# Performance work log

Hardware: AMD Instinct MI355X
Metric: run time of the kernel (lower is better)

Reference implementation:

```python
import jax, jax.numpy as jnp
import numpy as np

EPS = 1e-8
SMALL = 1e-3


def _skew(v):
    # v: [B,3] -> [B,3,3]
    vx, vy, vz = v[:, 0], v[:, 1], v[:, 2]
    z = jnp.zeros_like(vx)
    row0 = jnp.stack([z, -vz, vy], axis=-1)
    row1 = jnp.stack([vz, z, -vx], axis=-1)
    row2 = jnp.stack([-vy, vx, z], axis=-1)
    return jnp.stack([row0, row1, row2], axis=-2)


def rotmat_axis_angle_stable(aa):
    # aa: [B,3] axis*angle -> [B,3,3], Taylor-stable near theta=0
    theta = jnp.linalg.norm(aa, axis=1)
    theta2 = theta * theta + EPS
    A = jnp.sin(theta) / (theta + EPS)
    Bc = (1.0 - jnp.cos(theta)) / theta2
    th2 = theta * theta
    th4 = th2 * th2
    small = theta < SMALL
    A = jnp.where(small, 1.0 - th2 / 6.0 + th4 / 120.0, A)
    Bc = jnp.where(small, 0.5 - th2 / 24.0 + th4 / 720.0, Bc)
    K = _skew(aa)
    I = jnp.eye(3, dtype=aa.dtype)
    return I + A[:, None, None] * K + Bc[:, None, None] * jnp.matmul(K, K)


def _euler_to_rot(rpy):
    # rpy: [J,3] -> [J,3,3] (URDF origin rotations, constants)
    r, p, y = rpy[:, 0], rpy[:, 1], rpy[:, 2]
    cr, sr = jnp.cos(r), jnp.sin(r)
    cp, sp = jnp.cos(p), jnp.sin(p)
    cy, sy = jnp.cos(y), jnp.sin(y)
    row0 = jnp.stack([cy * cp, cy * sp * sr - sy * cr, cy * sp * cr + sy * sr], -1)
    row1 = jnp.stack([sy * cp, sy * sp * sr + cy * cr, sy * sp * cr - cy * sr], -1)
    row2 = jnp.stack([-sp, cp * sr, cp * cr], -1)
    return jnp.stack([row0, row1, row2], axis=-2)


def setup_inputs() -> dict:
    key = jax.random.key(0)
    k1, k2, k3, k4 = jax.random.split(key, 4)
    B, J = 131072, 24
    joint_angles = jax.random.normal(k1, (B, J), dtype=jnp.float32)
    # URDF origin constants: small offsets + rotations per joint
    xyz = 0.1 * jax.random.normal(k2, (J, 3), dtype=jnp.float32)
    rpy = 0.3 * jax.random.normal(k3, (J, 3), dtype=jnp.float32)
    R = _euler_to_rot(rpy)                                      # [J,3,3]
    T_origins = jnp.tile(jnp.eye(4, dtype=jnp.float32), (J, 1, 1))
    T_origins = T_origins.at[:, :3, :3].set(R).at[:, :3, 3].set(xyz)
    ax = jax.random.normal(k4, (J, 3), dtype=jnp.float32)
    axes = ax / jnp.linalg.norm(ax, axis=1, keepdims=True)      # unit axes
    return {"joint_angles": joint_angles, "T_origins": T_origins, "axes": axes}


def reference(joint_angles, T_origins, axes) -> jnp.ndarray:
    # joint_angles: [B,J]; T_origins: [J,4,4]; axes: [J,3]
    joint_angles = joint_angles.astype(jnp.float32)
    B = joint_angles.shape[0]
    eye4 = jnp.eye(4, dtype=jnp.float32)

    def step(T_parent, xs):
        T_org, axis, ang = xs                     # [4,4], [3], [B]
        aa = axis[None, :] * ang[:, None]         # [B,3]
        Rj = rotmat_axis_angle_stable(aa)         # [B,3,3]
        Tj = jnp.broadcast_to(eye4, (B, 4, 4)).at[:, :3, :3].set(Rj)
        T_child = jnp.matmul(jnp.matmul(T_parent, T_org), Tj)   # [B,4,4]
        return T_child, T_child[:, :3, 3]

    T0 = jnp.broadcast_to(eye4, (B, 4, 4))
    xs = (T_origins, axes, joint_angles.T)        # scan over J joints
    _, pos = jax.lax.scan(step, T0, xs)           # pos: [J,B,3]
    base_pos = jnp.zeros((B, 3), dtype=jnp.float32)
    pos = jnp.transpose(pos, (1, 0, 2)).reshape(B, -1)          # [B,J*3]
    return jnp.concatenate([base_pos, pos], axis=1)             # [B,(J+1)*3]
```

## Files before the change

### kernel.cpp

```cpp
#include <hip/hip_runtime.h>

#define BLK 256
#define NJ 24
#define G 8
#define NG (NJ / G)

typedef float vf4 __attribute__((ext_vector_type(4)));

__global__ __launch_bounds__(BLK, 2)
void fk_kernel(const float* __restrict__ angles,
               const float* __restrict__ Torg,
               const float* __restrict__ axes,
               float* __restrict__ out,
               int B)
{
    __shared__ float stage[BLK * 75];
    __shared__ float sQK[NJ * 8];
    __shared__ float sAx[NJ * 4];

    const int tid = threadIdx.x;
    const int b = blockIdx.x * BLK + tid;

    const float4* ap = reinterpret_cast<const float4*>(angles + (size_t)b * NJ);
    const float4 av0 = ap[0], av1 = ap[1], av2 = ap[2];
    const float4 av3 = ap[3], av4 = ap[4], av5 = ap[5];

    if (tid < NJ) {
        const float* o = Torg + tid * 16;
        const float m00=o[0], m01=o[1], m02=o[2];
        const float m10=o[4], m11=o[5], m12=o[6];
        const float m20=o[8], m21=o[9], m22=o[10];
        const float tr = m00 + m11 + m22;
        float qw, qx, qy, qz;
        if (tr > 0.f) {
            const float S = sqrtf(tr + 1.f) * 2.f;
            qw = 0.25f * S;
            qx = (m21 - m12) / S;
            qy = (m02 - m20) / S;
            qz = (m10 - m01) / S;
        } else if (m00 > m11 && m00 > m22) {
            const float S = sqrtf(1.f + m00 - m11 - m22) * 2.f;
            qw = (m21 - m12) / S;
            qx = 0.25f * S;
            qy = (m01 + m10) / S;
            qz = (m02 + m20) / S;
        } else if (m11 > m22) {
            const float S = sqrtf(1.f + m11 - m00 - m22) * 2.f;
            qw = (m02 - m20) / S;
            qx = (m01 + m10) / S;
            qy = 0.25f * S;
            qz = (m12 + m21) / S;
        } else {
            const float S = sqrtf(1.f + m22 - m00 - m11) * 2.f;
            qw = (m10 - m01) / S;
            qx = (m02 + m20) / S;
            qy = (m12 + m21) / S;
            qz = 0.25f * S;
        }
        float* q = &sQK[tid * 8];
        q[0] = qw; q[1] = qx; q[2] = qy; q[3] = qz;
        q[4] = o[3]; q[5] = o[7]; q[6] = o[11]; q[7] = 0.f;
        float* ax = &sAx[tid * 4];
        ax[0] = axes[tid*3+0]; ax[1] = axes[tid*3+1]; ax[2] = axes[tid*3+2]; ax[3] = 0.f;
    }
    __syncthreads();

    float Qw = 1.f, Qx = 0.f, Qy = 0.f, Qz = 0.f;
    float tx = 0.f, ty = 0.f, tz = 0.f;

    float* srow = &stage[tid * 75];
    srow[0] = 0.f; srow[1] = 0.f; srow[2] = 0.f;

    #pragma unroll 1
    for (int g = 0; g < NG; ++g) {
        float a[G];
        if (g == 0) {
            a[0]=av0.x; a[1]=av0.y; a[2]=av0.z; a[3]=av0.w;
            a[4]=av1.x; a[5]=av1.y; a[6]=av1.z; a[7]=av1.w;
        } else if (g == 1) {
            a[0]=av2.x; a[1]=av2.y; a[2]=av2.z; a[3]=av2.w;
            a[4]=av3.x; a[5]=av3.y; a[6]=av3.z; a[7]=av3.w;
        } else {
            a[0]=av4.x; a[1]=av4.y; a[2]=av4.z; a[3]=av4.w;
            a[4]=av5.x; a[5]=av5.y; a[6]=av5.z; a[7]=av5.w;
        }

        float U[G][4];
        float OT[G][3];
        #pragma unroll
        for (int u = 0; u < G; ++u) {
            const int j = g * G + u;
            const float4 qo = *reinterpret_cast<const float4*>(&sQK[j*8]);
            const float4 ot = *reinterpret_cast<const float4*>(&sQK[j*8+4]);
            const float4 ax = *reinterpret_cast<const float4*>(&sAx[j*4]);
            OT[u][0] = ot.x; OT[u][1] = ot.y; OT[u][2] = ot.z;

            const float h = 0.5f * a[u];
            const float s = __sinf(h);
            const float c = __cosf(h);
            const float bx = s * ax.x, by = s * ax.y, bz = s * ax.z;

            U[u][0] = qo.x*c  - qo.y*bx - qo.z*by - qo.w*bz;
            U[u][1] = qo.x*bx + qo.y*c  + qo.z*bz - qo.w*by;
            U[u][2] = qo.x*by - qo.y*bz + qo.z*c  + qo.w*bx;
            U[u][3] = qo.x*bz + qo.y*by - qo.z*bx + qo.w*c;
        }

        #pragma unroll
        for (int u = 0; u < G; ++u) {
            const int j = g * G + u;
            const float ox = OT[u][0], oy = OT[u][1], oz = OT[u][2];

            const float cx = Qy*oz - Qz*oy + Qw*ox;
            const float cy = Qz*ox - Qx*oz + Qw*oy;
            const float cz = Qx*oy - Qy*ox + Qw*oz;
            const float dx = Qy*cz - Qz*cy;
            const float dy = Qz*cx - Qx*cz;
            const float dz = Qx*cy - Qy*cx;
            tx = tx + ox + 2.f*dx;
            ty = ty + oy + 2.f*dy;
            tz = tz + oz + 2.f*dz;

            const float uw = U[u][0], ux = U[u][1], uy = U[u][2], uz = U[u][3];
            const float nw = Qw*uw - Qx*ux - Qy*uy - Qz*uz;
            const float nx = Qw*ux + Qx*uw + Qy*uz - Qz*uy;
            const float ny = Qw*uy - Qx*uz + Qy*uw + Qz*ux;
            const float nz = Qw*uz + Qx*uy - Qy*ux + Qz*uw;
            Qw = nw; Qx = nx; Qy = ny; Qz = nz;

            srow[3 + 3*j + 0] = tx;
            srow[3 + 3*j + 1] = ty;
            srow[3 + 3*j + 2] = tz;
        }
    }

    __syncthreads();

    vf4* out4 = reinterpret_cast<vf4*>(out + (size_t)blockIdx.x * BLK * 75);
    const vf4* st4 = reinterpret_cast<const vf4*>(stage);
    #pragma unroll
    for (int k = 0; k < 18; ++k) {
        const vf4 v = st4[tid + k * BLK];
        __builtin_nontemporal_store(v, &out4[tid + k * BLK]);
    }
    if (tid < (BLK * 75 / 4) - 18 * BLK) {
        const vf4 v = st4[tid + 18 * BLK];
        __builtin_nontemporal_store(v, &out4[tid + 18 * BLK]);
    }
}

extern "C" void kernel_launch(void* const* d_in, const int* in_sizes, int n_in,
                              void* d_out, int out_size, void* d_ws, size_t ws_size,
                              hipStream_t stream) {
    const float* angles = (const float*)d_in[0];
    const float* Torg   = (const float*)d_in[1];
    const float* axes   = (const float*)d_in[2];
    float* out = (float*)d_out;

    const int B = in_sizes[0] / NJ;
    const int grid = (B + BLK - 1) / BLK;

    fk_kernel<<<grid, BLK, 0, stream>>>(angles, Torg, axes, out, B);
}
```

Measured before the change: 19.13 us.

## Precompute origin-axis quaternion products per wave and drop block barriers

Each wave now computes its own copy of the per-joint constants, so the block-wide barrier after setup can be removed. The origin quaternion times axis quaternion product is precomputed, which turns each joint rotation into c*P + s*Q instead of a full quaternion multiply. The output copy from shared memory is split so each wave writes its own 64 rows, removing the final block barrier. In exchange, the setup work is repeated in every wave and shared memory use grows slightly.

New measurement: 17.82 us. 1.07x faster.

```diff
diff --git a/kernel.cpp b/kernel.cpp
--- a/kernel.cpp
+++ b/kernel.cpp
@@ -4,6 +4,7 @@
 #define NJ 24
 #define G 8
 #define NG (NJ / G)
+#define NWV (BLK / 64)
 
 typedef float vf4 __attribute__((ext_vector_type(4)));
 
@@ -15,18 +16,21 @@
                int B)
 {
     __shared__ float stage[BLK * 75];
-    __shared__ float sQK[NJ * 8];
-    __shared__ float sAx[NJ * 4];
+    __shared__ float sP[NWV][NJ * 4];
+    __shared__ float sQ[NWV][NJ * 4];
+    __shared__ float sOT[NWV][NJ * 4];
 
-    const int tid = threadIdx.x;
-    const int b = blockIdx.x * BLK + tid;
+    const int tid  = threadIdx.x;
+    const int lane = tid & 63;
+    const int wv   = tid >> 6;
+    const int b    = blockIdx.x * BLK + tid;
 
     const float4* ap = reinterpret_cast<const float4*>(angles + (size_t)b * NJ);
     const float4 av0 = ap[0], av1 = ap[1], av2 = ap[2];
     const float4 av3 = ap[3], av4 = ap[4], av5 = ap[5];
 
-    if (tid < NJ) {
-        const float* o = Torg + tid * 16;
+    if (lane < NJ) {
+        const float* o = Torg + lane * 16;
         const float m00=o[0], m01=o[1], m02=o[2];
         const float m10=o[4], m11=o[5], m12=o[6];
         const float m20=o[8], m21=o[9], m22=o[10];
@@ -57,13 +61,19 @@
             qy = (m12 + m21) / S;
             qz = 0.25f * S;
         }
-        float* q = &sQK[tid * 8];
-        q[0] = qw; q[1] = qx; q[2] = qy; q[3] = qz;
-        q[4] = o[3]; q[5] = o[7]; q[6] = o[11]; q[7] = 0.f;
-        float* ax = &sAx[tid * 4];
-        ax[0] = axes[tid*3+0]; ax[1] = axes[tid*3+1]; ax[2] = axes[tid*3+2]; ax[3] = 0.f;
+        const float axx = axes[lane*3+0], axy = axes[lane*3+1], axz = axes[lane*3+2];
+        const float Qw_ = -qx*axx - qy*axy - qz*axz;
+        const float Qx_ =  qw*axx + qy*axz - qz*axy;
+        const float Qy_ =  qw*axy - qx*axz + qz*axx;
+        const float Qz_ =  qw*axz + qx*axy - qy*axx;
+
+        float* p = &sP[wv][lane * 4];
+        p[0] = qw; p[1] = qx; p[2] = qy; p[3] = qz;
+        float* q = &sQ[wv][lane * 4];
+        q[0] = Qw_; q[1] = Qx_; q[2] = Qy_; q[3] = Qz_;
+        float* t = &sOT[wv][lane * 4];
+        t[0] = o[3]; t[1] = o[7]; t[2] = o[11]; t[3] = 0.f;
     }
-    __syncthreads();
 
     float Qw = 1.f, Qx = 0.f, Qy = 0.f, Qz = 0.f;
     float tx = 0.f, ty = 0.f, tz = 0.f;
@@ -90,20 +100,19 @@
         #pragma unroll
         for (int u = 0; u < G; ++u) {
             const int j = g * G + u;
-            const float4 qo = *reinterpret_cast<const float4*>(&sQK[j*8]);
-            const float4 ot = *reinterpret_cast<const float4*>(&sQK[j*8+4]);
-            const float4 ax = *reinterpret_cast<const float4*>(&sAx[j*4]);
+            const float4 P  = *reinterpret_cast<const float4*>(&sP[wv][j*4]);
+            const float4 Qv = *reinterpret_cast<const float4*>(&sQ[wv][j*4]);
+            const float4 ot = *reinterpret_cast<const float4*>(&sOT[wv][j*4]);
             OT[u][0] = ot.x; OT[u][1] = ot.y; OT[u][2] = ot.z;
 
             const float h = 0.5f * a[u];
             const float s = __sinf(h);
             const float c = __cosf(h);
-            const float bx = s * ax.x, by = s * ax.y, bz = s * ax.z;
 
-            U[u][0] = qo.x*c  - qo.y*bx - qo.z*by - qo.w*bz;
-            U[u][1] = qo.x*bx + qo.y*c  + qo.z*bz - qo.w*by;
-            U[u][2] = qo.x*by - qo.y*bz + qo.z*c  + qo.w*bx;
-            U[u][3] = qo.x*bz + qo.y*by - qo.z*bx + qo.w*c;
+            U[u][0] = c*P.x + s*Qv.x;
+            U[u][1] = c*P.y + s*Qv.y;
+            U[u][2] = c*P.z + s*Qv.z;
+            U[u][3] = c*P.w + s*Qv.w;
         }
 
         #pragma unroll
@@ -134,18 +143,20 @@
         }
     }
 
-    __syncthreads();
-
-    vf4* out4 = reinterpret_cast<vf4*>(out + (size_t)blockIdx.x * BLK * 75);
-    const vf4* st4 = reinterpret_cast<const vf4*>(stage);
-    #pragma unroll
-    for (int k = 0; k < 18; ++k) {
-        const vf4 v = st4[tid + k * BLK];
-        __builtin_nontemporal_store(v, &out4[tid + k * BLK]);
-    }
-    if (tid < (BLK * 75 / 4) - 18 * BLK) {
-        const vf4 v = st4[tid + 18 * BLK];
-        __builtin_nontemporal_store(v, &out4[tid + 18 * BLK]);
+    {
+        const int rowbase = wv * 64;
+        float* obase = out + ((size_t)blockIdx.x * BLK + rowbase) * 75;
+        vf4* out4 = reinterpret_cast<vf4*>(obase);
+        const vf4* st4 = reinterpret_cast<const vf4*>(&stage[rowbase * 75]);
+        #pragma unroll
+        for (int k = 0; k < 18; ++k) {
+            const vf4 v = st4[lane + k * 64];
+            __builtin_nontemporal_store(v, &out4[lane + k * 64]);
+        }
+        if (lane < 1200 - 18 * 64) {
+            const vf4 v = st4[lane + 18 * 64];
+            __builtin_nontemporal_store(v, &out4[lane + 18 * 64]);
+        }
     }
 }
 
```
